# Performance work log

Measured on AMD Instinct MI355X. Metric: run time of the kernel, lower is better.

The kernel has to match this reference:

```python
import jax, jax.numpy as jnp
import numpy as np

SEQ_DIM = 256
PAIR_DIM = 128
N_HEADS = 8
HIDDEN = 32
B, L = 4, 512


def layer_norm(x, gamma, beta, eps=1e-5):
    mu = jnp.mean(x, axis=-1, keepdims=True)
    var = jnp.var(x, axis=-1, keepdims=True)
    return (x - mu) * jax.lax.rsqrt(var + eps) * gamma + beta


def setup_inputs() -> dict:
    key = jax.random.key(0)
    ks = jax.random.split(key, 12)
    d = N_HEADS * HIDDEN
    s = 0.02
    return {
        "seq": jax.random.normal(ks[0], (B, L, SEQ_DIM), jnp.float32),
        "pair": jax.random.normal(ks[1], (B, L, L, PAIR_DIM), jnp.float32),
        "ln_seq_g": jnp.ones((SEQ_DIM,), jnp.float32),
        "ln_seq_b": jnp.zeros((SEQ_DIM,), jnp.float32),
        "ln_pair_g": jnp.ones((PAIR_DIM,), jnp.float32),
        "ln_pair_b": jnp.zeros((PAIR_DIM,), jnp.float32),
        "W_b": jax.random.normal(ks[2], (PAIR_DIM, N_HEADS), jnp.float32) * s,
        "W_q": jax.random.normal(ks[3], (SEQ_DIM, d), jnp.float32) * s,
        "W_k": jax.random.normal(ks[4], (SEQ_DIM, d), jnp.float32) * s,
        "W_v": jax.random.normal(ks[5], (SEQ_DIM, d), jnp.float32) * s,
        "W_g": jax.random.normal(ks[6], (SEQ_DIM, d), jnp.float32) * s,
        "b_g": jnp.zeros((d,), jnp.float32),
        "W_o": jax.random.normal(ks[7], (d, SEQ_DIM), jnp.float32) * s,
        "b_o": jnp.zeros((SEQ_DIM,), jnp.float32),
    }


def reference(seq, pair, ln_seq_g, ln_seq_b, ln_pair_g, ln_pair_b,
              W_b, W_q, W_k, W_v, W_g, b_g, W_o, b_o):
    b, l, _ = seq.shape
    factor = 1.0 / np.sqrt(HIDDEN).astype(np.float32)
    s = layer_norm(seq, ln_seq_g, ln_seq_b)
    p = layer_norm(pair, ln_pair_g, ln_pair_b)
    Q = (s @ W_q).reshape(b, l, N_HEADS, HIDDEN)
    K = (s @ W_k).reshape(b, l, N_HEADS, HIDDEN)
    V = (s @ W_v).reshape(b, l, N_HEADS, HIDDEN)
    # pair bias: [b, i, j, n] -> [b, n, i, j]
    bias = jnp.einsum('bijp,pn->bnij', p, W_b)
    att = jnp.einsum('binh,bjnh->bnij', Q, K) * factor + bias
    att = jax.nn.softmax(att, axis=-1)
    gate = jax.nn.sigmoid(s @ W_g + b_g).reshape(b, l, N_HEADS, HIDDEN)
    out = jnp.einsum('bnij,bjnh->binh', att, V) * gate
    out = out.reshape(b, l, N_HEADS * HIDDEN)
    return out @ W_o + b_o
```

## Files before the change

### kernel.cpp

```cpp
#include <hip/hip_runtime.h>
#include <math.h>

#define OFF_Q    0
#define OFF_K    (524288)
#define OFF_V    (524288*2)
#define OFF_G    (524288*3)
#define OFF_PRE  (524288*4)
#define OFF_BIAS (524288*5)

template <int CTRL>
__device__ __forceinline__ float dpp_mov(float x) {
  return __int_as_float(__builtin_amdgcn_update_dpp(0, __float_as_int(x), CTRL, 0xF, 0xF, true));
}
template <int CTRL>
__device__ __forceinline__ float dpp_add(float x) { return x + dpp_mov<CTRL>(x); }
__device__ __forceinline__ float red16(float v) {
  v = dpp_add<0xB1>(v);
  v = dpp_add<0x4E>(v);
  v = dpp_add<0x141>(v);
  v = dpp_add<0x140>(v);
  return v;
}

#define SEL8(a, f, out) do { \
  float _s0 = ((f)&1) ? a[1] : a[0]; \
  float _s1 = ((f)&1) ? a[3] : a[2]; \
  float _s2 = ((f)&1) ? a[5] : a[4]; \
  float _s3 = ((f)&1) ? a[7] : a[6]; \
  float _t0 = ((f)&2) ? _s1 : _s0; \
  float _t1 = ((f)&2) ? _s3 : _s2; \
  out = ((f)&4) ? _t1 : _t0; \
} while(0)

__device__ __forceinline__ float4 sel8_f4(const float4* a, int f) {
  float4 s0 = (f&1) ? a[1] : a[0];
  float4 s1 = (f&1) ? a[3] : a[2];
  float4 s2 = (f&1) ? a[5] : a[4];
  float4 s3 = (f&1) ? a[7] : a[6];
  float4 t0 = (f&2) ? s1 : s0;
  float4 t1 = (f&2) ? s3 : s2;
  return (f&4) ? t1 : t0;
}

__device__ __forceinline__ float dot4(float4 a, float4 b, float acc) {
  acc = fmaf(a.x, b.x, acc); acc = fmaf(a.y, b.y, acc);
  acc = fmaf(a.z, b.z, acc); return fmaf(a.w, b.w, acc);
}

template <int CTRL>
__device__ __forceinline__ void merge_dpp(float& m, float& l, float4* acc) {
  float m2 = dpp_mov<CTRL>(m);
  float l2 = dpp_mov<CTRL>(l);
  float M = fmaxf(m, m2);
  float ea = __expf(m - M), eb = __expf(m2 - M);
  l = l*ea + l2*eb;
#pragma unroll
  for (int x = 0; x < 8; ++x) {
    acc[x].x = acc[x].x*ea + dpp_mov<CTRL>(acc[x].x)*eb;
    acc[x].y = acc[x].y*ea + dpp_mov<CTRL>(acc[x].y)*eb;
    acc[x].z = acc[x].z*ea + dpp_mov<CTRL>(acc[x].z)*eb;
    acc[x].w = acc[x].w*ea + dpp_mov<CTRL>(acc[x].w)*eb;
  }
  m = M;
}

__global__ __launch_bounds__(256, 3) void k_mega(
    const float* __restrict__ seq, const float* __restrict__ lsg, const float* __restrict__ lsb,
    const float* __restrict__ lpg, const float* __restrict__ lpb, const float* __restrict__ Wb,
    const float* __restrict__ Wq, const float* __restrict__ Wk, const float* __restrict__ Wv,
    const float* __restrict__ Wg, const float* __restrict__ bg, const float* __restrict__ pair,
    float* __restrict__ Qw, float* __restrict__ Kw, float* __restrict__ Vw, float* __restrict__ Gw,
    float* __restrict__ biasw) {
  __shared__ __align__(16) float As[256*36];
  int t = threadIdx.x;
  int blk = blockIdx.x;

  if (blk < 512) {
    int m0 = (blk >> 3) * 32;
    int y = blk & 7;
    {
      int r = t >> 3, c0 = t & 7;
      const float* srow = seq + (size_t)(m0 + r) * 256;
      float4 v[8];
      float s = 0.f, sq = 0.f;
#pragma unroll
      for (int qq = 0; qq < 8; ++qq) {
        v[qq] = *(const float4*)(srow + 4*(c0 + 8*qq));
        s += v[qq].x + v[qq].y + v[qq].z + v[qq].w;
        sq = fmaf(v[qq].x, v[qq].x, sq); sq = fmaf(v[qq].y, v[qq].y, sq);
        sq = fmaf(v[qq].z, v[qq].z, sq); sq = fmaf(v[qq].w, v[qq].w, sq);
      }
#pragma unroll
      for (int mm = 1; mm < 8; mm <<= 1) { s += __shfl_xor(s, mm); sq += __shfl_xor(sq, mm); }
      float mu = s * (1.f/256.f);
      float var = sq * (1.f/256.f) - mu*mu;
      float rstd = rsqrtf(var + 1e-5f);
#pragma unroll
      for (int qq = 0; qq < 8; ++qq) {
        int c4 = c0 + 8*qq;
        float4 g  = *(const float4*)(lsg + 4*c4);
        float4 bb = *(const float4*)(lsb + 4*c4);
        float* dp = As + 4*c4*36 + r;
        dp[0]   = (v[qq].x - mu)*rstd*g.x + bb.x;
        dp[36]  = (v[qq].y - mu)*rstd*g.y + bb.y;
        dp[72]  = (v[qq].z - mu)*rstd*g.z + bb.z;
        dp[108] = (v[qq].w - mu)*rstd*g.w + bb.w;
      }
    }
    __syncthreads();
    const float* Wm = (y < 2) ? Wq : (y < 4) ? Wk : (y < 6) ? Wv : Wg;
    int cb = (y & 1) * 128;
    int rg = t >> 5, cg2 = t & 31;
    const float* bp = Wm + cb + 4*cg2;
    const float* ap = As + 4*rg;
    float4 a0 = {0,0,0,0}, a1 = {0,0,0,0}, a2 = {0,0,0,0}, a3 = {0,0,0,0};
#pragma unroll 4
    for (int p = 0; p < 256; ++p) {
      float4 a  = *(const float4*)(ap + p*36);
      float4 bv = *(const float4*)(bp + p*256);
      a0.x = fmaf(a.x, bv.x, a0.x); a0.y = fmaf(a.x, bv.y, a0.y);
      a0.z = fmaf(a.x, bv.z, a0.z); a0.w = fmaf(a.x, bv.w, a0.w);
      a1.x = fmaf(a.y, bv.x, a1.x); a1.y = fmaf(a.y, bv.y, a1.y);
      a1.z = fmaf(a.y, bv.z, a1.z); a1.w = fmaf(a.y, bv.w, a1.w);
      a2.x = fmaf(a.z, bv.x, a2.x); a2.y = fmaf(a.z, bv.y, a2.y);
      a2.z = fmaf(a.z, bv.z, a2.z); a2.w = fmaf(a.z, bv.w, a2.w);
      a3.x = fmaf(a.w, bv.x, a3.x); a3.y = fmaf(a.w, bv.y, a3.y);
      a3.z = fmaf(a.w, bv.z, a3.z); a3.w = fmaf(a.w, bv.w, a3.w);
    }
    int mat = y >> 1;
    int col = cb + 4*cg2;
    float* outp = (mat == 0) ? Qw : (mat == 1) ? Kw : (mat == 2) ? Vw : Gw;
    if (mat == 0) {
      const float qs = 0.17677669529663687f;
      a0.x*=qs; a0.y*=qs; a0.z*=qs; a0.w*=qs;
      a1.x*=qs; a1.y*=qs; a1.z*=qs; a1.w*=qs;
      a2.x*=qs; a2.y*=qs; a2.z*=qs; a2.w*=qs;
      a3.x*=qs; a3.y*=qs; a3.z*=qs; a3.w*=qs;
    }
    if (mat == 3) {
      float4 g4 = *(const float4*)(bg + col);
      a0.x = 1.f/(1.f+__expf(-(a0.x+g4.x))); a0.y = 1.f/(1.f+__expf(-(a0.y+g4.y)));
      a0.z = 1.f/(1.f+__expf(-(a0.z+g4.z))); a0.w = 1.f/(1.f+__expf(-(a0.w+g4.w)));
      a1.x = 1.f/(1.f+__expf(-(a1.x+g4.x))); a1.y = 1.f/(1.f+__expf(-(a1.y+g4.y)));
      a1.z = 1.f/(1.f+__expf(-(a1.z+g4.z))); a1.w = 1.f/(1.f+__expf(-(a1.w+g4.w)));
      a2.x = 1.f/(1.f+__expf(-(a2.x+g4.x))); a2.y = 1.f/(1.f+__expf(-(a2.y+g4.y)));
      a2.z = 1.f/(1.f+__expf(-(a2.z+g4.z))); a2.w = 1.f/(1.f+__expf(-(a2.w+g4.w)));
      a3.x = 1.f/(1.f+__expf(-(a3.x+g4.x))); a3.y = 1.f/(1.f+__expf(-(a3.y+g4.y)));
      a3.z = 1.f/(1.f+__expf(-(a3.z+g4.z))); a3.w = 1.f/(1.f+__expf(-(a3.w+g4.w)));
    }
    int orow = m0 + 4*rg;
    *(float4*)(outp + (size_t)(orow+0)*256 + col) = a0;
    *(float4*)(outp + (size_t)(orow+1)*256 + col) = a1;
    *(float4*)(outp + (size_t)(orow+2)*256 + col) = a2;
    *(float4*)(outp + (size_t)(orow+3)*256 + col) = a3;
    return;
  }

  int bb2 = blk - 512;
  int b = bb2 >> 9, i = bb2 & 511;
  int lane = t & 63, w = t >> 6;
  int grp = lane >> 4, f = lane & 15;

  float wp[64];
  float cg[8] = {0,0,0,0,0,0,0,0}, cbv[8] = {0,0,0,0,0,0,0,0};
#pragma unroll
  for (int q = 0; q < 4; ++q) {
    int kA = 4*f + q, kB = 64 + 4*f + q;
    float gA = lpg[kA], bA = lpb[kA];
    float gB = lpg[kB], bB = lpb[kB];
    float4 uA0 = *(const float4*)(Wb + kA*8);
    float4 uA1 = *(const float4*)(Wb + kA*8 + 4);
    float4 uB0 = *(const float4*)(Wb + kB*8);
    float4 uB1 = *(const float4*)(Wb + kB*8 + 4);
    wp[q*8+0] = gA*uA0.x; cg[0] += wp[q*8+0]; cbv[0] = fmaf(bA, uA0.x, cbv[0]);
    wp[q*8+1] = gA*uA0.y; cg[1] += wp[q*8+1]; cbv[1] = fmaf(bA, uA0.y, cbv[1]);
    wp[q*8+2] = gA*uA0.z; cg[2] += wp[q*8+2]; cbv[2] = fmaf(bA, uA0.z, cbv[2]);
    wp[q*8+3] = gA*uA0.w; cg[3] += wp[q*8+3]; cbv[3] = fmaf(bA, uA0.w, cbv[3]);
    wp[q*8+4] = gA*uA1.x; cg[4] += wp[q*8+4]; cbv[4] = fmaf(bA, uA1.x, cbv[4]);
    wp[q*8+5] = gA*uA1.y; cg[5] += wp[q*8+5]; cbv[5] = fmaf(bA, uA1.y, cbv[5]);
    wp[q*8+6] = gA*uA1.z; cg[6] += wp[q*8+6]; cbv[6] = fmaf(bA, uA1.z, cbv[6]);
    wp[q*8+7] = gA*uA1.w; cg[7] += wp[q*8+7]; cbv[7] = fmaf(bA, uA1.w, cbv[7]);
    int qb8 = (4+q)*8;
    wp[qb8+0] = gB*uB0.x; cg[0] += wp[qb8+0]; cbv[0] = fmaf(bB, uB0.x, cbv[0]);
    wp[qb8+1] = gB*uB0.y; cg[1] += wp[qb8+1]; cbv[1] = fmaf(bB, uB0.y, cbv[1]);
    wp[qb8+2] = gB*uB0.z; cg[2] += wp[qb8+2]; cbv[2] = fmaf(bB, uB0.z, cbv[2]);
    wp[qb8+3] = gB*uB0.w; cg[3] += wp[qb8+3]; cbv[3] = fmaf(bB, uB0.w, cbv[3]);
    wp[qb8+4] = gB*uB1.x; cg[4] += wp[qb8+4]; cbv[4] = fmaf(bB, uB1.x, cbv[4]);
    wp[qb8+5] = gB*uB1.y; cg[5] += wp[qb8+5]; cbv[5] = fmaf(bB, uB1.y, cbv[5]);
    wp[qb8+6] = gB*uB1.z; cg[6] += wp[qb8+6]; cbv[6] = fmaf(bB, uB1.z, cbv[6]);
    wp[qb8+7] = gB*uB1.w; cg[7] += wp[qb8+7]; cbv[7] = fmaf(bB, uB1.w, cbv[7]);
  }
#pragma unroll
  for (int n2 = 0; n2 < 8; ++n2) { cg[n2] = red16(cg[n2]); cbv[n2] = red16(cbv[n2]); }
  float cgsel, cbsel;
  SEL8(cg, f, cgsel);
  SEL8(cbv, f, cbsel);

  const float* prow0 = pair + (size_t)(b*512 + i) * (512*128);
  float* bw0 = biasw + (size_t)(b*512 + i) * 512 * 8;

  int j0 = 4*w + grp;
  const float* rp = prow0 + (size_t)j0*128 + 4*f;

#define PROCROW(X0, X1, JJ) { \
    float s_  = X0.x + X0.y + X0.z + X0.w + X1.x + X1.y + X1.z + X1.w; \
    float sq_ = X0.x*X0.x; \
    sq_ = fmaf(X0.y, X0.y, sq_); sq_ = fmaf(X0.z, X0.z, sq_); sq_ = fmaf(X0.w, X0.w, sq_); \
    sq_ = fmaf(X1.x, X1.x, sq_); sq_ = fmaf(X1.y, X1.y, sq_); \
    sq_ = fmaf(X1.z, X1.z, sq_); sq_ = fmaf(X1.w, X1.w, sq_); \
    float dd_[8]; \
    _Pragma("unroll") \
    for (int n2 = 0; n2 < 8; ++n2) { \
      float d_ = X0.x * wp[n2]; \
      d_ = fmaf(X0.y, wp[8+n2],  d_); \
      d_ = fmaf(X0.z, wp[16+n2], d_); \
      d_ = fmaf(X0.w, wp[24+n2], d_); \
      d_ = fmaf(X1.x, wp[32+n2], d_); \
      d_ = fmaf(X1.y, wp[40+n2], d_); \
      d_ = fmaf(X1.z, wp[48+n2], d_); \
      d_ = fmaf(X1.w, wp[56+n2], d_); \
      dd_[n2] = d_; \
    } \
    s_  = red16(s_); \
    sq_ = red16(sq_); \
    _Pragma("unroll") \
    for (int n2 = 0; n2 < 8; ++n2) dd_[n2] = red16(dd_[n2]); \
    float mu_ = s_ * (1.f/128.f); \
    float var_ = fmaf(sq_, 1.f/128.f, -mu_*mu_); \
    float rstd_ = rsqrtf(var_ + 1e-5f); \
    if (f < 8) { \
      float dv_; \
      SEL8(dd_, f, dv_); \
      bw0[(size_t)(JJ)*8 + f] = fmaf(rstd_, fmaf(-mu_, cgsel, dv_), cbsel); \
    } \
  }

  float4 A0[4], A1[4], B0[4], B1[4];
#pragma unroll
  for (int q = 0; q < 4; ++q) {
    const float* r = rp + (size_t)q*2048;
    A0[q] = *(const float4*)r; A1[q] = *(const float4*)(r + 64);
  }
#pragma unroll
  for (int q = 0; q < 4; ++q) {
    const float* r = rp + (size_t)(4+q)*2048;
    B0[q] = *(const float4*)r; B1[q] = *(const float4*)(r + 64);
  }

#define CHUNK(C0, C1, cc) { \
    _Pragma("unroll") \
    for (int q = 0; q < 4; ++q) PROCROW(C0[q], C1[q], (j0 + ((cc)*4 + q)*16)); \
    if ((cc) + 2 < 8) { \
      _Pragma("unroll") \
      for (int q = 0; q < 4; ++q) { \
        const float* r = rp + (size_t)(((cc)+2)*4 + q)*2048; \
        C0[q] = *(const float4*)r; C1[q] = *(const float4*)(r + 64); \
      } \
    } \
  }

  CHUNK(A0, A1, 0)
  CHUNK(B0, B1, 1)
  CHUNK(A0, A1, 2)
  CHUNK(B0, B1, 3)
  CHUNK(A0, A1, 4)
  CHUNK(B0, B1, 5)
  CHUNK(A0, A1, 6)
  CHUNK(B0, B1, 7)
#undef CHUNK
#undef PROCROW
}

__global__ __launch_bounds__(512) void k_attn5(
    const float* __restrict__ Qw, const float* __restrict__ Kw, const float* __restrict__ Vw,
    const float* __restrict__ Gw, const float* __restrict__ biasw, float* __restrict__ prew) {
  __shared__ __align__(16) float Kb[2][32*292];
  __shared__ __align__(16) float Vb[2][32*292];
  float* scr = &Kb[0][0];

  int t = threadIdx.x, lane = t & 63, w = t >> 6;
  int b = blockIdx.x >> 6, i0 = (blockIdx.x & 63) << 3;
  int n = lane >> 3, js = lane & 7;
  int ip = w & 3, jset = w >> 2;
  int ila = 2*ip, ilb = ila + 1;
  size_t qra = (size_t)(b*512 + i0 + ila);
  size_t qrb = qra + 1;
  int jl0 = jset*16 + js;

  float4 qa[8], qb[8];
  {
    const float* pa = Qw + qra*256 + n*32;
    const float* pb = Qw + qrb*256 + n*32;
#pragma unroll
    for (int x = 0; x < 8; ++x) { qa[x] = *(const float4*)(pa + 4*x); qb[x] = *(const float4*)(pb + 4*x); }
  }
  float4 acca[8], accb[8];
#pragma unroll
  for (int x = 0; x < 8; ++x) { acca[x] = make_float4(0,0,0,0); accb[x] = make_float4(0,0,0,0); }
  float ma = -1e30f, la = 0.f, mb2 = -1e30f, lb2 = 0.f;

  const float* Kg = Kw + (size_t)(b*512)*256;
  const float* Vg = Vw + (size_t)(b*512)*256;
  const float* Bpa = biasw + ((size_t)(b*512 + i0 + ila)*512 + jl0)*8 + n;
  const float* Bpb = Bpa + 512*8;

  float4 sk[4], sv[4];
  int woff = (lane >> 3)*36 + (lane & 7)*4;

#define SLOAD(tn) { \
    const float* ks_ = Kg + ((size_t)(tn)*32 + 4*w)*256 + 4*lane; \
    const float* vs_ = Vg + ((size_t)(tn)*32 + 4*w)*256 + 4*lane; \
    sk[0] = *(const float4*)(ks_);       sk[1] = *(const float4*)(ks_ + 256); \
    sk[2] = *(const float4*)(ks_ + 512); sk[3] = *(const float4*)(ks_ + 768); \
    sv[0] = *(const float4*)(vs_);       sv[1] = *(const float4*)(vs_ + 256); \
    sv[2] = *(const float4*)(vs_ + 512); sv[3] = *(const float4*)(vs_ + 768); \
  }
#define SWRITE(tn) { int bf_ = (tn) & 1; \
    float* kd_ = &Kb[bf_][(4*w)*292 + woff]; \
    *(float4*)(kd_)       = sk[0]; *(float4*)(kd_ + 292) = sk[1]; \
    *(float4*)(kd_ + 584) = sk[2]; *(float4*)(kd_ + 876) = sk[3]; \
    float* vd_ = &Vb[bf_][(4*w)*292 + woff]; \
    *(float4*)(vd_)       = sv[0]; *(float4*)(vd_ + 292) = sv[1]; \
    *(float4*)(vd_ + 584) = sv[2]; *(float4*)(vd_ + 876) = sv[3]; \
  }

  SLOAD(0);
  SWRITE(0);
  __syncthreads();

  for (int tt = 0; tt < 16; ++tt) {
    int cur = tt & 1;
    if (tt < 15) SLOAD(tt+1);

    const float* Kt = Kb[cur];
    const float* Vt = Vb[cur];
    float bba0 = Bpa[tt*256], bba1 = Bpa[tt*256 + 64];
    float bbb0 = Bpb[tt*256], bbb1 = Bpb[tt*256 + 64];

    float lga0, lga1, lgb0, lgb1;
    {
      const float* kp = Kt + jl0*292 + n*36;
      float da = 0.f, db = 0.f;
#pragma unroll
      for (int x = 0; x < 8; ++x) {
        float4 kk = *(const float4*)(kp + 4*x);
        da = dot4(qa[x], kk, da); db = dot4(qb[x], kk, db);
      }
      lga0 = da + bba0; lgb0 = db + bbb0;
    }
    {
      const float* kp = Kt + (jl0+8)*292 + n*36;
      float da = 0.f, db = 0.f;
#pragma unroll
      for (int x = 0; x < 8; ++x) {
        float4 kk = *(const float4*)(kp + 4*x);
        da = dot4(qa[x], kk, da); db = dot4(qb[x], kk, db);
      }
      lga1 = da + bba1; lgb1 = db + bbb1;
    }
    {
      float tm = fmaxf(lga0, lga1);
      if (tm > ma) {
        float sc = __expf(ma - tm);
        la *= sc;
#pragma unroll
        for (int x = 0; x < 8; ++x) {
          acca[x].x *= sc; acca[x].y *= sc; acca[x].z *= sc; acca[x].w *= sc;
        }
        ma = tm;
      }
    }
    {
      float tm = fmaxf(lgb0, lgb1);
      if (tm > mb2) {
        float sc = __expf(mb2 - tm);
        lb2 *= sc;
#pragma unroll
        for (int x = 0; x < 8; ++x) {
          accb[x].x *= sc; accb[x].y *= sc; accb[x].z *= sc; accb[x].w *= sc;
        }
        mb2 = tm;
      }
    }
    float pa0 = __expf(lga0 - ma), pa1 = __expf(lga1 - ma);
    float pb0 = __expf(lgb0 - mb2), pb1 = __expf(lgb1 - mb2);
    la += pa0 + pa1; lb2 += pb0 + pb1;
    {
      const float* vp = Vt + jl0*292 + n*36;
#pragma unroll
      for (int x = 0; x < 8; ++x) {
        float4 vv = *(const float4*)(vp + 4*x);
        acca[x].x = fmaf(pa0, vv.x, acca[x].x); acca[x].y = fmaf(pa0, vv.y, acca[x].y);
        acca[x].z = fmaf(pa0, vv.z, acca[x].z); acca[x].w = fmaf(pa0, vv.w, acca[x].w);
        accb[x].x = fmaf(pb0, vv.x, accb[x].x); accb[x].y = fmaf(pb0, vv.y, accb[x].y);
        accb[x].z = fmaf(pb0, vv.z, accb[x].z); accb[x].w = fmaf(pb0, vv.w, accb[x].w);
      }
    }
    {
      const float* vp = Vt + (jl0+8)*292 + n*36;
#pragma unroll
      for (int x = 0; x < 8; ++x) {
        float4 vv = *(const float4*)(vp + 4*x);
        acca[x].x = fmaf(pa1, vv.x, acca[x].x); acca[x].y = fmaf(pa1, vv.y, acca[x].y);
        acca[x].z = fmaf(pa1, vv.z, acca[x].z); acca[x].w = fmaf(pa1, vv.w, acca[x].w);
        accb[x].x = fmaf(pb1, vv.x, accb[x].x); accb[x].y = fmaf(pb1, vv.y, accb[x].y);
        accb[x].z = fmaf(pb1, vv.z, accb[x].z); accb[x].w = fmaf(pb1, vv.w, accb[x].w);
      }
    }

    if (tt < 15) SWRITE(tt+1);
    __syncthreads();
  }
#undef SLOAD
#undef SWRITE

  merge_dpp<0xB1>(ma, la, acca);   merge_dpp<0xB1>(mb2, lb2, accb);
  merge_dpp<0x4E>(ma, la, acca);   merge_dpp<0x4E>(mb2, lb2, accb);
  merge_dpp<0x141>(ma, la, acca);  merge_dpp<0x141>(mb2, lb2, accb);

  float4 fa = sel8_f4(acca, js);
  float4 fb = sel8_f4(accb, js);

  if (jset == 1) {
    int base = (ip*8 + n)*68;
    *(float4*)(scr + base + 4*js) = fa;
    *(float4*)(scr + base + 32 + 4*js) = fb;
    if (js == 0) { scr[base+64] = ma; scr[base+65] = la; scr[base+66] = mb2; scr[base+67] = lb2; }
  }
  __syncthreads();
  if (jset == 0) {
    int base = (ip*8 + n)*68;
    float4 a2 = *(const float4*)(scr + base + 4*js);
    float4 b2 = *(const float4*)(scr + base + 32 + 4*js);
    float m2a = scr[base+64], l2a = scr[base+65];
    float m2b = scr[base+66], l2b = scr[base+67];
    {
      float M = fmaxf(ma, m2a);
      float ea = __expf(ma - M), eb = __expf(m2a - M);
      float inv = 1.f / (la*ea + l2a*eb);
      float4 g4 = *(const float4*)(Gw + qra*256 + n*32 + 4*js);
      float4 r;
      r.x = (fa.x*ea + a2.x*eb) * inv * g4.x;
      r.y = (fa.y*ea + a2.y*eb) * inv * g4.y;
      r.z = (fa.z*ea + a2.z*eb) * inv * g4.z;
      r.w = (fa.w*ea + a2.w*eb) * inv * g4.w;
      *(float4*)(prew + qra*256 + n*32 + 4*js) = r;
    }
    {
      float M = fmaxf(mb2, m2b);
      float ea = __expf(mb2 - M), eb = __expf(m2b - M);
      float inv = 1.f / (lb2*ea + l2b*eb);
      float4 g4 = *(const float4*)(Gw + qrb*256 + n*32 + 4*js);
      float4 r;
      r.x = (fb.x*ea + b2.x*eb) * inv * g4.x;
      r.y = (fb.y*ea + b2.y*eb) * inv * g4.y;
      r.z = (fb.z*ea + b2.z*eb) * inv * g4.z;
      r.w = (fb.w*ea + b2.w*eb) * inv * g4.w;
      *(float4*)(prew + qrb*256 + n*32 + 4*js) = r;
    }
  }
}

__global__ __launch_bounds__(256) void k_out(
    const float* __restrict__ prew, const float* __restrict__ Wo, const float* __restrict__ bo,
    float* __restrict__ out) {
  __shared__ __align__(16) float As[256*36];
  int t = threadIdx.x;
  int m0 = blockIdx.x * 32;
  int y = blockIdx.y;
  {
    int r = t >> 3, c0 = t & 7;
    const float* srow = prew + (size_t)(m0 + r)*256;
#pragma unroll
    for (int qq = 0; qq < 8; ++qq) {
      int c4 = c0 + 8*qq;
      float4 v = *(const float4*)(srow + 4*c4);
      float* dp = As + 4*c4*36 + r;
      dp[0] = v.x; dp[36] = v.y; dp[72] = v.z; dp[108] = v.w;
    }
  }
  __syncthreads();
  int cb = y*128;
  int rg = t >> 5, cg2 = t & 31;
  int col = cb + 4*cg2;
  const float* bp = Wo + col;
  const float* ap = As + 4*rg;
  float4 a0 = {0,0,0,0}, a1 = {0,0,0,0}, a2 = {0,0,0,0}, a3 = {0,0,0,0};
#pragma unroll 4
  for (int p = 0; p < 256; ++p) {
    float4 a  = *(const float4*)(ap + p*36);
    float4 bv = *(const float4*)(bp + p*256);
    a0.x = fmaf(a.x, bv.x, a0.x); a0.y = fmaf(a.x, bv.y, a0.y);
    a0.z = fmaf(a.x, bv.z, a0.z); a0.w = fmaf(a.x, bv.w, a0.w);
    a1.x = fmaf(a.y, bv.x, a1.x); a1.y = fmaf(a.y, bv.y, a1.y);
    a1.z = fmaf(a.y, bv.z, a1.z); a1.w = fmaf(a.y, bv.w, a1.w);
    a2.x = fmaf(a.z, bv.x, a2.x); a2.y = fmaf(a.z, bv.y, a2.y);
    a2.z = fmaf(a.z, bv.z, a2.z); a2.w = fmaf(a.z, bv.w, a2.w);
    a3.x = fmaf(a.w, bv.x, a3.x); a3.y = fmaf(a.w, bv.y, a3.y);
    a3.z = fmaf(a.w, bv.z, a3.z); a3.w = fmaf(a.w, bv.w, a3.w);
  }
  float4 b4 = *(const float4*)(bo + col);
  a0.x += b4.x; a0.y += b4.y; a0.z += b4.z; a0.w += b4.w;
  a1.x += b4.x; a1.y += b4.y; a1.z += b4.z; a1.w += b4.w;
  a2.x += b4.x; a2.y += b4.y; a2.z += b4.z; a2.w += b4.w;
  a3.x += b4.x; a3.y += b4.y; a3.z += b4.z; a3.w += b4.w;
  int orow = m0 + 4*rg;
  *(float4*)(out + (size_t)(orow+0)*256 + col) = a0;
  *(float4*)(out + (size_t)(orow+1)*256 + col) = a1;
  *(float4*)(out + (size_t)(orow+2)*256 + col) = a2;
  *(float4*)(out + (size_t)(orow+3)*256 + col) = a3;
}

extern "C" void kernel_launch(void* const* d_in, const int* in_sizes, int n_in,
                              void* d_out, int out_size, void* d_ws, size_t ws_size,
                              hipStream_t stream) {
  const float* seq  = (const float*)d_in[0];
  const float* pair = (const float*)d_in[1];
  const float* lsg  = (const float*)d_in[2];
  const float* lsb  = (const float*)d_in[3];
  const float* lpg  = (const float*)d_in[4];
  const float* lpb  = (const float*)d_in[5];
  const float* Wb   = (const float*)d_in[6];
  const float* Wq   = (const float*)d_in[7];
  const float* Wk   = (const float*)d_in[8];
  const float* Wv   = (const float*)d_in[9];
  const float* Wg   = (const float*)d_in[10];
  const float* bg   = (const float*)d_in[11];
  const float* Wo   = (const float*)d_in[12];
  const float* bo   = (const float*)d_in[13];
  float* ws   = (float*)d_ws;
  float* Qw   = ws + OFF_Q;
  float* Kw   = ws + OFF_K;
  float* Vw   = ws + OFF_V;
  float* Gw   = ws + OFF_G;
  float* prew = ws + OFF_PRE;
  float* biasw= ws + OFF_BIAS;
  float* out  = (float*)d_out;

  hipLaunchKernelGGL(k_mega, dim3(2560), dim3(256), 0, stream,
                     seq, lsg, lsb, lpg, lpb, Wb, Wq, Wk, Wv, Wg, bg, pair,
                     Qw, Kw, Vw, Gw, biasw);
  hipLaunchKernelGGL(k_attn5, dim3(256), dim3(512), 0, stream,
                     Qw, Kw, Vw, Gw, biasw, prew);
  hipLaunchKernelGGL(k_out, dim3(64, 2), dim3(256), 0, stream,
                     prew, Wo, bo, out);
}
```

Before: 205.7 us.

## Make pair-bias blocks persistent with strided row loop and put them first

The pair layer-norm and bias projection now runs on 512 long-lived blocks instead of 2048 blocks, one per (b,i) row. Each 16-lane group walks the flattened pair rows with a large stride over 32 double-buffered chunks, so the per-block weight and gamma/beta setup is paid fewer times. These pair blocks now come first in the grid and the Q/K/V/G projection blocks come after them. The risk is lower occupancy, since 512 blocks may not fill every CU slot, which could reduce memory parallelism on this bandwidth-bound stream. The chunk loop is also no longer fully unrolled.

```diff
diff --git a/kernel.cpp b/kernel.cpp
--- a/kernel.cpp
+++ b/kernel.cpp
@@ -75,9 +75,10 @@
   int t = threadIdx.x;
   int blk = blockIdx.x;
 
-  if (blk < 512) {
-    int m0 = (blk >> 3) * 32;
-    int y = blk & 7;
+  if (blk >= 512) {
+    int kb = blk - 512;
+    int m0 = (kb >> 3) * 32;
+    int y = kb & 7;
     {
       int r = t >> 3, c0 = t & 7;
       const float* srow = seq + (size_t)(m0 + r) * 256;
@@ -156,8 +157,6 @@
     return;
   }
 
-  int bb2 = blk - 512;
-  int b = bb2 >> 9, i = bb2 & 511;
   int lane = t & 63, w = t >> 6;
   int grp = lane >> 4, f = lane & 15;
 
@@ -196,13 +195,11 @@
   SEL8(cg, f, cgsel);
   SEL8(cbv, f, cbsel);
 
-  const float* prow0 = pair + (size_t)(b*512 + i) * (512*128);
-  float* bw0 = biasw + (size_t)(b*512 + i) * 512 * 8;
-
-  int j0 = 4*w + grp;
-  const float* rp = prow0 + (size_t)j0*128 + 4*f;
-
-#define PROCROW(X0, X1, JJ) { \
+  int gid = blk*16 + w*4 + grp;
+  const float* rp0 = pair + (size_t)gid*128 + 4*f;
+  float* bw0 = biasw + (size_t)gid*8 + f;
+
+#define PROCROW(X0, X1, IDX) { \
     float s_  = X0.x + X0.y + X0.z + X0.w + X1.x + X1.y + X1.z + X1.w; \
     float sq_ = X0.x*X0.x; \
     sq_ = fmaf(X0.y, X0.y, sq_); sq_ = fmaf(X0.z, X0.z, sq_); sq_ = fmaf(X0.w, X0.w, sq_); \
@@ -231,42 +228,38 @@
     if (f < 8) { \
       float dv_; \
       SEL8(dd_, f, dv_); \
-      bw0[(size_t)(JJ)*8 + f] = fmaf(rstd_, fmaf(-mu_, cgsel, dv_), cbsel); \
+      bw0[(size_t)(IDX)*65536] = fmaf(rstd_, fmaf(-mu_, cgsel, dv_), cbsel); \
     } \
   }
 
   float4 A0[4], A1[4], B0[4], B1[4];
 #pragma unroll
   for (int q = 0; q < 4; ++q) {
-    const float* r = rp + (size_t)q*2048;
+    const float* r = rp0 + (size_t)q*1048576;
     A0[q] = *(const float4*)r; A1[q] = *(const float4*)(r + 64);
   }
 #pragma unroll
   for (int q = 0; q < 4; ++q) {
-    const float* r = rp + (size_t)(4+q)*2048;
+    const float* r = rp0 + (size_t)(4+q)*1048576;
     B0[q] = *(const float4*)r; B1[q] = *(const float4*)(r + 64);
   }
 
 #define CHUNK(C0, C1, cc) { \
     _Pragma("unroll") \
-    for (int q = 0; q < 4; ++q) PROCROW(C0[q], C1[q], (j0 + ((cc)*4 + q)*16)); \
-    if ((cc) + 2 < 8) { \
+    for (int q = 0; q < 4; ++q) PROCROW(C0[q], C1[q], (4*(cc) + q)); \
+    if ((cc) + 2 < 32) { \
       _Pragma("unroll") \
       for (int q = 0; q < 4; ++q) { \
-        const float* r = rp + (size_t)(((cc)+2)*4 + q)*2048; \
+        const float* r = rp0 + (size_t)(4*((cc)+2) + q)*1048576; \
         C0[q] = *(const float4*)r; C1[q] = *(const float4*)(r + 64); \
       } \
     } \
   }
 
-  CHUNK(A0, A1, 0)
-  CHUNK(B0, B1, 1)
-  CHUNK(A0, A1, 2)
-  CHUNK(B0, B1, 3)
-  CHUNK(A0, A1, 4)
-  CHUNK(B0, B1, 5)
-  CHUNK(A0, A1, 6)
-  CHUNK(B0, B1, 7)
+  for (int c = 0; c < 32; c += 2) {
+    CHUNK(A0, A1, c)
+    CHUNK(B0, B1, c+1)
+  }
 #undef CHUNK
 #undef PROCROW
 }
@@ -537,7 +530,7 @@
   float* biasw= ws + OFF_BIAS;
   float* out  = (float*)d_out;
 
-  hipLaunchKernelGGL(k_mega, dim3(2560), dim3(256), 0, stream,
+  hipLaunchKernelGGL(k_mega, dim3(1024), dim3(256), 0, stream,
                      seq, lsg, lsb, lpg, lpb, Wb, Wq, Wk, Wv, Wg, bg, pair,
                      Qw, Kw, Vw, Gw, biasw);
   hipLaunchKernelGGL(k_attn5, dim3(256), dim3(512), 0, stream,
```

Result: no change. 205.7 us (-0.0%).
